# Performance work log

Hardware: AMD Instinct MI355X
Metric: run time of the kernel (lower is better)

## Reference

```python
import jax, jax.numpy as jnp
import numpy as np

B, S, D, H = 2, 2048, 1024, 16
DK = D // H


def setup_inputs() -> dict:
    key = jax.random.key(0)
    ks = jax.random.split(key, 6)
    inp = {
        "mha_input": jax.random.normal(ks[0], (B, S, D), dtype=jnp.float32),
        "mask": jax.random.randint(ks[1], (B, S), 0, 2, dtype=jnp.int32),
        "Wq_w": jax.random.normal(ks[2], (D, D), dtype=jnp.float32) * 0.02,
        "Wq_b": jnp.zeros((D,), dtype=jnp.float32),
        "Wk_w": jax.random.normal(ks[3], (D, D), dtype=jnp.float32) * 0.02,
        "Wk_b": jnp.zeros((D,), dtype=jnp.float32),
        "Wv_w": jax.random.normal(ks[4], (D, D), dtype=jnp.float32) * 0.02,
        "Wv_b": jnp.zeros((D,), dtype=jnp.float32),
        "Wo_w": jax.random.normal(ks[5], (D, D), dtype=jnp.float32) * 0.02,
        "Wo_b": jnp.zeros((D,), dtype=jnp.float32),
    }
    return inp


def _mha(x, mask, Wq_w, Wq_b, Wk_w, Wk_b, Wv_w, Wv_b, Wo_w, Wo_b):
    b, s, d = x.shape
    # nn.Linear: x @ W.T + b
    q = (x @ Wq_w.T + Wq_b).reshape(b, s, H, DK).transpose(0, 2, 1, 3)  # [B,H,S,DK]
    k = (x @ Wk_w.T + Wk_b).reshape(b, s, H, DK).transpose(0, 2, 1, 3)
    v = (x @ Wv_w.T + Wv_b).reshape(b, s, H, DK).transpose(0, 2, 1, 3)
    scores = jnp.einsum("bhqd,bhkd->bhqk", q, k) / jnp.sqrt(jnp.float32(DK))
    # prefix mask: key columns < count_nonzero(mask[i]) are kept, rest -inf
    lengths = jnp.count_nonzero(mask, axis=1)                # [B]
    valid = jnp.arange(s)[None, :] < lengths[:, None]        # [B,S]
    scores = jnp.where(valid[:, None, None, :], scores, -jnp.inf)
    attn = jax.nn.softmax(scores, axis=-1)
    out = jnp.einsum("bhqk,bhkd->bhqd", attn, v)             # [B,H,S,DK]
    concat = out.transpose(0, 2, 1, 3).reshape(b, s, d)      # [B,S,D]
    return concat @ Wo_w.T + Wo_b


def reference(mha_input, mask, Wq_w, Wq_b, Wk_w, Wk_b, Wv_w, Wv_b, Wo_w, Wo_b):
    return _mha(mha_input, mask, Wq_w, Wq_b, Wk_w, Wk_b, Wv_w, Wv_b, Wo_w, Wo_b)
```

## Files before the change

kernel.cpp:

```cpp
#include <hip/hip_runtime.h>

using bf16x8 = __attribute__((ext_vector_type(8))) short;
using f32x4  = __attribute__((ext_vector_type(4))) float;

#define S_LEN 2048
#define NHEAD 16
#define DKH   64
#define HSZ   (S_LEN * DKH * 32)
#define QSCALE 0.18033688011112042f

#if __has_builtin(__builtin_amdgcn_exp2f)
#define EXP2(x) __builtin_amdgcn_exp2f(x)
#else
#define EXP2(x) exp2f(x)
#endif

__device__ __forceinline__ unsigned short f2bf(float x) {
  unsigned u = __builtin_bit_cast(unsigned, x);
  u += 0x7FFFu + ((u >> 16) & 1u);
  return (unsigned short)(u >> 16);
}

__device__ __forceinline__ void gload_lds16(const void* g, void* l) {
  __builtin_amdgcn_global_load_lds(
      (const __attribute__((address_space(1))) unsigned int*)g,
      (__attribute__((address_space(3))) unsigned int*)l, 16, 0, 0);
}

__global__ void cvt_kernel(const float* __restrict__ src,
                           unsigned short* __restrict__ dst, int n4) {
  int i = blockIdx.x * blockDim.x + threadIdx.x;
  if (i < n4) {
    float4 v = ((const float4*)src)[i];
    ushort4 o;
    o.x = f2bf(v.x); o.y = f2bf(v.y); o.z = f2bf(v.z); o.w = f2bf(v.w);
    ((ushort4*)dst)[i] = o;
  }
}

__global__ void lens_kernel(const int* __restrict__ mask, int* __restrict__ lens) {
  __shared__ int sred[256];
  const int b = blockIdx.x;
  int c = 0;
  for (int s = threadIdx.x; s < S_LEN; s += 256) c += (mask[b * S_LEN + s] != 0) ? 1 : 0;
  sred[threadIdx.x] = c;
  __syncthreads();
  for (int st = 128; st > 0; st >>= 1) {
    if (threadIdx.x < st) sred[threadIdx.x] += sred[threadIdx.x + st];
    __syncthreads();
  }
  if (threadIdx.x == 0) lens[b] = sred[0];
}

template <int MODE>
__global__ __launch_bounds__(256) void gemm_kernel(
    const unsigned short* __restrict__ A, const unsigned short* __restrict__ B,
    const float* __restrict__ b0, const float* __restrict__ b1,
    const float* __restrict__ b2, unsigned short* __restrict__ outQKV,
    float* __restrict__ outF, const int K) {
  __shared__ __align__(16) unsigned short As[128 * 32];
  __shared__ __align__(16) unsigned short Bs[128 * 32];
  const int tid = threadIdx.x;
  const int w = tid >> 6, lane = tid & 63;
  const int wm = w >> 1, wn = w & 1;
  const int r = lane & 15, g = lane >> 4;
  const int tm = blockIdx.y * 128, tn = blockIdx.x * 128;

  f32x4 acc[4][4] = {};
  const char* Ab = (const char*)A;
  const char* Bb = (const char*)B;
  char* AsB = (char*)As;
  char* BsB = (char*)Bs;

  for (int k0 = 0; k0 < K; k0 += 32) {
#pragma unroll
    for (int i = 0; i < 2; ++i) {
      const int o = (w * 2 + i) * 1024 + lane * 16;
      const int row = o >> 6, colb = o & 63;
      gload_lds16(Ab + ((size_t)(tm + row) * K + k0) * 2 + colb, AsB + (w * 2 + i) * 1024);
      gload_lds16(Bb + ((size_t)(tn + row) * K + k0) * 2 + colb, BsB + (w * 2 + i) * 1024);
    }
    __syncthreads();
    bf16x8 af[4], bfr[4];
#pragma unroll
    for (int mi = 0; mi < 4; ++mi)
      af[mi] = *(const bf16x8*)(AsB + (wm * 64 + mi * 16 + r) * 64 + g * 16);
#pragma unroll
    for (int ni = 0; ni < 4; ++ni)
      bfr[ni] = *(const bf16x8*)(BsB + (wn * 64 + ni * 16 + r) * 64 + g * 16);
#pragma unroll
    for (int mi = 0; mi < 4; ++mi)
#pragma unroll
      for (int ni = 0; ni < 4; ++ni)
        acc[mi][ni] = __builtin_amdgcn_mfma_f32_16x16x32_bf16(af[mi], bfr[ni], acc[mi][ni], 0, 0, 0);
    __syncthreads();
  }

  if (MODE == 0) {
    const int mat = tn >> 10;
    const float* bp = (mat == 0) ? b0 : (mat == 1) ? b1 : b2;
    const float scale = (mat == 0) ? QSCALE : 1.0f;
    unsigned short* dst = outQKV + (size_t)mat * HSZ;
#pragma unroll
    for (int mi = 0; mi < 4; ++mi)
#pragma unroll
      for (int ni = 0; ni < 4; ++ni)
#pragma unroll
        for (int reg = 0; reg < 4; ++reg) {
          const int m = tm + wm * 64 + mi * 16 + 4 * g + reg;
          const int n = tn + wn * 64 + ni * 16 + r;
          const int nn = n & 1023;
          const float v = (acc[mi][ni][reg] + bp[nn]) * scale;
          const int bI = m >> 11, s = m & 2047, hh = nn >> 6, dk = nn & 63;
          if (mat == 2) {
            dst[(size_t)((bI * NHEAD + hh) * DKH + dk) * S_LEN + s] = f2bf(v);
          } else {
            dst[(size_t)((bI * NHEAD + hh) * S_LEN + s) * DKH + dk] = f2bf(v);
          }
        }
  } else {
#pragma unroll
    for (int mi = 0; mi < 4; ++mi)
#pragma unroll
      for (int ni = 0; ni < 4; ++ni)
#pragma unroll
        for (int reg = 0; reg < 4; ++reg) {
          const int m = tm + wm * 64 + mi * 16 + 4 * g + reg;
          const int n = tn + wn * 64 + ni * 16 + r;
          outF[(size_t)m * 1024 + n] = acc[mi][ni][reg] + b0[n];
        }
  }
}

__device__ __forceinline__ void online_sm(f32x4* st, float& mrun, float& lrun,
                                          f32x4* oacc, int g) {
  float mloc = st[0][0];
#pragma unroll
  for (int f = 0; f < 4; ++f)
#pragma unroll
    for (int q = 0; q < 4; ++q) mloc = fmaxf(mloc, st[f][q]);
  mloc = fmaxf(mloc, __shfl_xor(mloc, 16));
  mloc = fmaxf(mloc, __shfl_xor(mloc, 32));
  const float mnew = fmaxf(mrun, mloc);
  const float alpha = EXP2(mrun - mnew);
  mrun = mnew;
  float psum = 0.f;
#pragma unroll
  for (int f = 0; f < 4; ++f)
#pragma unroll
    for (int q = 0; q < 4; ++q) {
      const float p = EXP2(st[f][q] - mnew);
      st[f][q] = p;
      psum += p;
    }
  psum += __shfl_xor(psum, 16);
  psum += __shfl_xor(psum, 32);
  lrun = lrun * alpha + psum;
  float areg[4];
#pragma unroll
  for (int q = 0; q < 4; ++q) areg[q] = __shfl(alpha, 4 * g + q);
#pragma unroll
  for (int f = 0; f < 4; ++f)
#pragma unroll
    for (int q = 0; q < 4; ++q) oacc[f][q] *= areg[q];
}

__global__ __launch_bounds__(256) void attn_kernel(
    const unsigned short* __restrict__ qkv, const int* __restrict__ lens,
    unsigned short* __restrict__ outc) {
  __shared__ __align__(16) unsigned short Kt[2][4096];
  __shared__ __align__(16) unsigned short Vt[2][4096];
  __shared__ __align__(16) unsigned short Pl[4][2][1024];
  const int tid = threadIdx.x;
  const int w = tid >> 6, lane = tid & 63;
  const int r = lane & 15, g = lane >> 4;
  const int bh = blockIdx.y;
  const int b = bh >> 4, h = bh & 15;
  const int q0 = blockIdx.x * 128;

  const unsigned short* Qp = qkv;
  const unsigned short* Kp = qkv + HSZ;
  const unsigned short* VTp = qkv + 2 * (size_t)HSZ;

  const size_t qbase = (size_t)(bh * S_LEN + q0 + w * 32 + r) * DKH;
  const bf16x8 qa0 = *(const bf16x8*)(Qp + qbase + g * 8);
  const bf16x8 qa1 = *(const bf16x8*)(Qp + qbase + 32 + g * 8);
  const bf16x8 qb0 = *(const bf16x8*)(Qp + qbase + 16 * DKH + g * 8);
  const bf16x8 qb1 = *(const bf16x8*)(Qp + qbase + 16 * DKH + 32 + g * 8);

  const int L = lens[b];
  const int nt = (L + 63) >> 6;
  float mA = -__builtin_inff(), lA = 0.f;
  float mB = -__builtin_inff(), lB = 0.f;
  f32x4 oA[4] = {}, oB[4] = {};

  char* PA = (char*)Pl[w][0];
  char* PB = (char*)Pl[w][1];
  const int swp = (r & 7) << 4;

  const char* kgb0 = (const char*)(Kp + (size_t)bh * S_LEN * DKH);
  const char* vgb0 = (const char*)(VTp + (size_t)bh * DKH * S_LEN);

  auto stage = [&](int tt, int bb) {
    const char* kgb = kgb0 + (size_t)tt * 64 * DKH * 2;
    const char* vgb = vgb0 + (size_t)tt * 64 * 2;
    char* kd = (char*)Kt[bb];
    char* vd = (char*)Vt[bb];
#pragma unroll
    for (int i = 0; i < 2; ++i) {
      const int o = i * 4096 + w * 1024 + lane * 16;
      const int row = o >> 7, colb = o & 127;
      const int cs = colb ^ ((row & 7) << 4);
      gload_lds16(kgb + row * 128 + cs, kd + i * 4096 + w * 1024);
      gload_lds16(vgb + (size_t)row * (S_LEN * 2) + cs, vd + i * 4096 + w * 1024);
    }
  };

  if (nt > 0) stage(0, 0);
  __syncthreads();

  int buf = 0;
  for (int t = 0; t < nt; ++t) {
    if (t + 1 < nt) stage(t + 1, buf ^ 1);

    const char* KtB = (const char*)Kt[buf];
    f32x4 sa[4], sb[4];
    __builtin_amdgcn_s_setprio(1);
#pragma unroll
    for (int f = 0; f < 4; ++f) {
      const int c = f * 16 + r;
      const int sw = (c & 7) << 4;
      const bf16x8 k0 = *(const bf16x8*)(KtB + c * 128 + ((g * 16) ^ sw));
      const bf16x8 k1 = *(const bf16x8*)(KtB + c * 128 + ((64 + g * 16) ^ sw));
      f32x4 x = {};
      x = __builtin_amdgcn_mfma_f32_16x16x32_bf16(k0, qa0, x, 0, 0, 0);
      x = __builtin_amdgcn_mfma_f32_16x16x32_bf16(k1, qa1, x, 0, 0, 0);
      sa[f] = x;
      f32x4 y = {};
      y = __builtin_amdgcn_mfma_f32_16x16x32_bf16(k0, qb0, y, 0, 0, 0);
      y = __builtin_amdgcn_mfma_f32_16x16x32_bf16(k1, qb1, y, 0, 0, 0);
      sb[f] = y;
    }
    __builtin_amdgcn_s_setprio(0);

    const int kv0 = t * 64;
    if (t == nt - 1) {
#pragma unroll
      for (int f = 0; f < 4; ++f)
#pragma unroll
        for (int q = 0; q < 4; ++q)
          if (kv0 + f * 16 + 4 * g + q >= L) {
            sa[f][q] = -__builtin_inff();
            sb[f][q] = -__builtin_inff();
          }
    }

    online_sm(sa, mA, lA, oA, g);
    online_sm(sb, mB, lB, oB, g);

#pragma unroll
    for (int f = 0; f < 4; ++f) {
      ushort4 pw;
      pw.x = f2bf(sa[f][0]); pw.y = f2bf(sa[f][1]);
      pw.z = f2bf(sa[f][2]); pw.w = f2bf(sa[f][3]);
      *(ushort4*)(PA + r * 128 + ((f * 32 + g * 8) ^ swp)) = pw;
      ushort4 qw;
      qw.x = f2bf(sb[f][0]); qw.y = f2bf(sb[f][1]);
      qw.z = f2bf(sb[f][2]); qw.w = f2bf(sb[f][3]);
      *(ushort4*)(PB + r * 128 + ((f * 32 + g * 8) ^ swp)) = qw;
    }

    const char* VtB = (const char*)Vt[buf];
#pragma unroll
    for (int c2 = 0; c2 < 2; ++c2) {
      const bf16x8 pa = *(const bf16x8*)(PA + r * 128 + ((c2 * 64 + g * 16) ^ swp));
      const bf16x8 pb = *(const bf16x8*)(PB + r * 128 + ((c2 * 64 + g * 16) ^ swp));
      __builtin_amdgcn_s_setprio(1);
#pragma unroll
      for (int f = 0; f < 4; ++f) {
        const int dk = f * 16 + r;
        const bf16x8 vf =
            *(const bf16x8*)(VtB + dk * 128 + ((c2 * 64 + g * 16) ^ ((dk & 7) << 4)));
        oA[f] = __builtin_amdgcn_mfma_f32_16x16x32_bf16(pa, vf, oA[f], 0, 0, 0);
        oB[f] = __builtin_amdgcn_mfma_f32_16x16x32_bf16(pb, vf, oB[f], 0, 0, 0);
      }
      __builtin_amdgcn_s_setprio(0);
    }

    __syncthreads();
    buf ^= 1;
  }

  const float iA = 1.0f / lA;
  const float iB = 1.0f / lB;
  float rA[4], rB[4];
#pragma unroll
  for (int q = 0; q < 4; ++q) {
    rA[q] = __shfl(iA, 4 * g + q);
    rB[q] = __shfl(iB, 4 * g + q);
  }
#pragma unroll
  for (int f = 0; f < 4; ++f) {
    const int dk = f * 16 + r;
#pragma unroll
    for (int q = 0; q < 4; ++q) {
      const int rowA = q0 + w * 32 + 4 * g + q;
      outc[(size_t)(b * S_LEN + rowA) * 1024 + h * DKH + dk] = f2bf(oA[f][q] * rA[q]);
      const int rowB = rowA + 16;
      outc[(size_t)(b * S_LEN + rowB) * 1024 + h * DKH + dk] = f2bf(oB[f][q] * rB[q]);
    }
  }
}

extern "C" void kernel_launch(void* const* d_in, const int* in_sizes, int n_in,
                              void* d_out, int out_size, void* d_ws, size_t ws_size,
                              hipStream_t stream) {
  const float* x  = (const float*)d_in[0];
  const int* mask = (const int*)d_in[1];
  const float* wq = (const float*)d_in[2];
  const float* bq = (const float*)d_in[3];
  const float* wk = (const float*)d_in[4];
  const float* bk = (const float*)d_in[5];
  const float* wv = (const float*)d_in[6];
  const float* bv = (const float*)d_in[7];
  const float* wo = (const float*)d_in[8];
  const float* bo = (const float*)d_in[9];
  (void)in_sizes; (void)n_in; (void)out_size; (void)ws_size;

  char* ws = (char*)d_ws;
  unsigned short* xb  = (unsigned short*)ws;
  unsigned short* wb  = (unsigned short*)(ws + 8388608);
  unsigned short* wob = (unsigned short*)(ws + 14680064);
  unsigned short* qkv = (unsigned short*)(ws + 16777216);
  unsigned short* ao  = (unsigned short*)(ws + 41943040);
  int* lens           = (int*)(ws + 50331648);
  float* out          = (float*)d_out;

  cvt_kernel<<<4096, 256, 0, stream>>>(x, xb, 1048576);
  cvt_kernel<<<1024, 256, 0, stream>>>(wq, wb, 262144);
  cvt_kernel<<<1024, 256, 0, stream>>>(wk, wb + 1048576, 262144);
  cvt_kernel<<<1024, 256, 0, stream>>>(wv, wb + 2097152, 262144);
  cvt_kernel<<<1024, 256, 0, stream>>>(wo, wob, 262144);
  lens_kernel<<<2, 256, 0, stream>>>(mask, lens);

  gemm_kernel<0><<<dim3(24, 32), 256, 0, stream>>>(xb, wb, bq, bk, bv, qkv, nullptr, 1024);
  attn_kernel<<<dim3(16, 32), 256, 0, stream>>>(qkv, lens, ao);
  gemm_kernel<1><<<dim3(8, 32), 256, 0, stream>>>(ao, wob, bo, nullptr, nullptr, nullptr, out, 1024);
}
```

Before: 216.6 us.

## Double-buffer GEMM LDS tiles and fuse conversion/length kernels into one launch

The GEMM main loop now double-buffers its A/B tiles in LDS, issuing the async global-to-LDS loads for the next k-tile before computing the current one. Explicit vmcnt waits and barriers replace the two __syncthreads per iteration. Separately, the five fp32-to-bf16 conversion launches and the mask length reduction are merged into a single kernel to cut launch overhead. This doubles GEMM LDS usage, which may lower occupancy, and relies on hand-placed waitcnt values being correct.

```diff
diff --git a/kernel.cpp b/kernel.cpp
--- a/kernel.cpp
+++ b/kernel.cpp
@@ -27,29 +27,52 @@
       (__attribute__((address_space(3))) unsigned int*)l, 16, 0, 0);
 }
 
-__global__ void cvt_kernel(const float* __restrict__ src,
-                           unsigned short* __restrict__ dst, int n4) {
-  int i = blockIdx.x * blockDim.x + threadIdx.x;
-  if (i < n4) {
-    float4 v = ((const float4*)src)[i];
-    ushort4 o;
-    o.x = f2bf(v.x); o.y = f2bf(v.y); o.z = f2bf(v.z); o.w = f2bf(v.w);
-    ((ushort4*)dst)[i] = o;
-  }
-}
-
-__global__ void lens_kernel(const int* __restrict__ mask, int* __restrict__ lens) {
+__global__ void cvt_lens_kernel(const float* __restrict__ x,
+                                const float* __restrict__ wq,
+                                const float* __restrict__ wk,
+                                const float* __restrict__ wv,
+                                const float* __restrict__ wo,
+                                const int* __restrict__ mask,
+                                unsigned short* __restrict__ xb,
+                                unsigned short* __restrict__ wb,
+                                unsigned short* __restrict__ wob,
+                                int* __restrict__ lens) {
   __shared__ int sred[256];
-  const int b = blockIdx.x;
-  int c = 0;
-  for (int s = threadIdx.x; s < S_LEN; s += 256) c += (mask[b * S_LEN + s] != 0) ? 1 : 0;
-  sred[threadIdx.x] = c;
-  __syncthreads();
-  for (int st = 128; st > 0; st >>= 1) {
-    if (threadIdx.x < st) sred[threadIdx.x] += sred[threadIdx.x + st];
+  if (blockIdx.x >= 8192) {
+    const int b = blockIdx.x - 8192;
+    int c = 0;
+    for (int s = threadIdx.x; s < S_LEN; s += 256) c += (mask[b * S_LEN + s] != 0) ? 1 : 0;
+    sred[threadIdx.x] = c;
     __syncthreads();
-  }
-  if (threadIdx.x == 0) lens[b] = sred[0];
+    for (int st = 128; st > 0; st >>= 1) {
+      if (threadIdx.x < st) sred[threadIdx.x] += sred[threadIdx.x + st];
+      __syncthreads();
+    }
+    if (threadIdx.x == 0) lens[b] = sred[0];
+    return;
+  }
+  const int i = blockIdx.x * 256 + threadIdx.x;
+  const float* s;
+  unsigned short* d;
+  if (i < 1048576) {
+    s = x + (size_t)i * 4;            d = xb + (size_t)i * 4;
+  } else if (i < 1310720) {
+    const int j = i - 1048576;
+    s = wq + (size_t)j * 4;           d = wb + (size_t)j * 4;
+  } else if (i < 1572864) {
+    const int j = i - 1310720;
+    s = wk + (size_t)j * 4;           d = wb + 1048576 + (size_t)j * 4;
+  } else if (i < 1835008) {
+    const int j = i - 1572864;
+    s = wv + (size_t)j * 4;           d = wb + 2097152 + (size_t)j * 4;
+  } else {
+    const int j = i - 1835008;
+    s = wo + (size_t)j * 4;           d = wob + (size_t)j * 4;
+  }
+  float4 v = *(const float4*)s;
+  ushort4 o;
+  o.x = f2bf(v.x); o.y = f2bf(v.y); o.z = f2bf(v.z); o.w = f2bf(v.w);
+  *(ushort4*)d = o;
 }
 
 template <int MODE>
@@ -58,8 +81,8 @@
     const float* __restrict__ b0, const float* __restrict__ b1,
     const float* __restrict__ b2, unsigned short* __restrict__ outQKV,
     float* __restrict__ outF, const int K) {
-  __shared__ __align__(16) unsigned short As[128 * 32];
-  __shared__ __align__(16) unsigned short Bs[128 * 32];
+  __shared__ __align__(16) unsigned short As[2][128 * 32];
+  __shared__ __align__(16) unsigned short Bs[2][128 * 32];
   const int tid = threadIdx.x;
   const int w = tid >> 6, lane = tid & 63;
   const int wm = w >> 1, wn = w & 1;
@@ -69,18 +92,35 @@
   f32x4 acc[4][4] = {};
   const char* Ab = (const char*)A;
   const char* Bb = (const char*)B;
-  char* AsB = (char*)As;
-  char* BsB = (char*)Bs;
-
-  for (int k0 = 0; k0 < K; k0 += 32) {
+  const int nk = K >> 5;
+
+  auto stage = [&](int kt, int bb) {
+    char* ad = (char*)As[bb];
+    char* bd = (char*)Bs[bb];
+    const int k0 = kt * 32;
 #pragma unroll
     for (int i = 0; i < 2; ++i) {
       const int o = (w * 2 + i) * 1024 + lane * 16;
       const int row = o >> 6, colb = o & 63;
-      gload_lds16(Ab + ((size_t)(tm + row) * K + k0) * 2 + colb, AsB + (w * 2 + i) * 1024);
-      gload_lds16(Bb + ((size_t)(tn + row) * K + k0) * 2 + colb, BsB + (w * 2 + i) * 1024);
-    }
-    __syncthreads();
+      gload_lds16(Ab + ((size_t)(tm + row) * K + k0) * 2 + colb, ad + (w * 2 + i) * 1024);
+      gload_lds16(Bb + ((size_t)(tn + row) * K + k0) * 2 + colb, bd + (w * 2 + i) * 1024);
+    }
+  };
+
+  stage(0, 0);
+  int buf = 0;
+  for (int kt = 0; kt < nk; ++kt) {
+    if (kt + 1 < nk) {
+      stage(kt + 1, buf ^ 1);
+      asm volatile("s_waitcnt vmcnt(4)" ::: "memory");
+    } else {
+      asm volatile("s_waitcnt vmcnt(0)" ::: "memory");
+    }
+    __builtin_amdgcn_s_barrier();
+    __builtin_amdgcn_sched_barrier(0);
+
+    const char* AsB = (const char*)As[buf];
+    const char* BsB = (const char*)Bs[buf];
     bf16x8 af[4], bfr[4];
 #pragma unroll
     for (int mi = 0; mi < 4; ++mi)
@@ -93,7 +133,11 @@
 #pragma unroll
       for (int ni = 0; ni < 4; ++ni)
         acc[mi][ni] = __builtin_amdgcn_mfma_f32_16x16x32_bf16(af[mi], bfr[ni], acc[mi][ni], 0, 0, 0);
-    __syncthreads();
+
+    asm volatile("s_waitcnt lgkmcnt(0)" ::: "memory");
+    __builtin_amdgcn_sched_barrier(0);
+    __builtin_amdgcn_s_barrier();
+    buf ^= 1;
   }
 
   if (MODE == 0) {
@@ -336,12 +380,7 @@
   int* lens           = (int*)(ws + 50331648);
   float* out          = (float*)d_out;
 
-  cvt_kernel<<<4096, 256, 0, stream>>>(x, xb, 1048576);
-  cvt_kernel<<<1024, 256, 0, stream>>>(wq, wb, 262144);
-  cvt_kernel<<<1024, 256, 0, stream>>>(wk, wb + 1048576, 262144);
-  cvt_kernel<<<1024, 256, 0, stream>>>(wv, wb + 2097152, 262144);
-  cvt_kernel<<<1024, 256, 0, stream>>>(wo, wob, 262144);
-  lens_kernel<<<2, 256, 0, stream>>>(mask, lens);
+  cvt_lens_kernel<<<8194, 256, 0, stream>>>(x, wq, wk, wv, wo, mask, xb, wb, wob, lens);
 
   gemm_kernel<0><<<dim3(24, 32), 256, 0, stream>>>(xb, wb, bq, bk, bv, qkv, nullptr, 1024);
   attn_kernel<<<dim3(16, 32), 256, 0, stream>>>(qkv, lens, ao);
```

Result: faster. 201.9 us (-6.8%).
